# Performance work log

Measured on AMD Instinct MI355X. Metric: run time of the kernel, lower is better.

## Reference

```python
import jax, jax.numpy as jnp
import numpy as np

N = 4096          # samples
D_FEAT = 256      # embedding dim
N_CLASSES = 64
N_NEIGHBORS = 3


def _sq_dists(x):
    # torch.cdist(x, x, p=2).pow(2): squared euclidean pairwise distances
    x2 = jnp.sum(x * x, axis=1)
    d = x2[:, None] + x2[None, :] - 2.0 * (x @ x.T)
    return jnp.maximum(d, 0.0)


def setup_inputs() -> dict:
    key = jax.random.key(0)
    k1, k2 = jax.random.split(key)
    outputs = jax.random.normal(k1, (N, D_FEAT), dtype=jnp.float32)
    label_inds = jax.random.randint(k2, (N,), 0, N_CLASSES)
    return {"outputs": outputs, "label_inds": label_inds, "n_neighbors": N_NEIGHBORS}


def reference(outputs, label_inds, n_neighbors):
    n = outputs.shape[0]
    D = _sq_dists(outputs)                                    # [n, n]

    # _select_targets: per-class k-NN == masked global k-NN (same squared dists)
    same = label_inds[:, None] == label_inds[None, :]
    eye = jnp.eye(n, dtype=bool)
    dd = jnp.where(same & ~eye, D, jnp.inf)
    _, tn = jax.lax.top_k(-dd, n_neighbors)                   # [n, k] target neighbors (global idx)

    target_d = jnp.take_along_axis(D, tn, axis=1)             # [n, k]
    pull = jnp.sum(target_d)
    margin_radii = 1.0 + jnp.max(target_d, axis=1)            # [n]

    # mask: True everywhere except target neighbors and the diagonal
    rows = jnp.arange(n)[:, None]
    mask = jnp.ones((n, n), dtype=bool).at[rows, tn].set(False) & ~eye

    # Original broadcast (max_dist [n,1] vs distance [n,1,n]) yields
    #   push = sum_i sum_{a,j} relu(margin_radii[i] - D[a,j]) * mask[a,j]
    # i.e. each r_i is compared against ALL masked distances. Compute this
    # O(n^3)-element sum exactly in O(n^2 log n) via sort + prefix sums:
    #   sum_d relu(r - d) = r * #{d < r} - sum_{d < r} d
    d_flat = jnp.where(mask.reshape(-1), D.reshape(-1), jnp.inf)
    d_sorted = jnp.sort(d_flat)
    csum = jnp.cumsum(jnp.where(jnp.isinf(d_sorted), 0.0, d_sorted))
    csum0 = jnp.concatenate([jnp.zeros((1,), D.dtype), csum])
    counts = jnp.searchsorted(d_sorted, margin_radii, side='left')  # strict d < r
    push = jnp.sum(margin_radii * counts.astype(D.dtype) - csum0[counts])

    return (pull + push) / n
```

## Files before the change

### kernel.cpp

```cpp
#include <hip/hip_runtime.h>
#include <hip/hip_bf16.h>
#include <float.h>

#define N 4096
#define DF 256
#define NBINS2 4096
#define MAXM 128
#define NPUSHBLK 528

typedef __attribute__((ext_vector_type(8))) short short8v;
typedef __attribute__((ext_vector_type(8))) unsigned short ushort8v;
typedef __attribute__((ext_vector_type(4))) float floatx4;

__device__ inline unsigned short f2bf(float f) {
    __hip_bfloat16 h = __float2bfloat16(f);
    return *reinterpret_cast<unsigned short*>(&h);
}
__device__ inline float bf2f(unsigned short h) {
    unsigned int u = ((unsigned int)h) << 16;
    return __uint_as_float(u);
}

__device__ inline void gload_lds16(const void* g, void* l) {
    __builtin_amdgcn_global_load_lds((const __attribute__((address_space(1))) void*)g,
                                     (__attribute__((address_space(3))) void*)l, 16, 0, 0);
}

__global__ __launch_bounds__(256) void prep_kernel(const float* __restrict__ X,
                                                   const int* __restrict__ labels,
                                                   float* __restrict__ x2,
                                                   __hip_bfloat16* __restrict__ Xb,
                                                   int* __restrict__ cnt,
                                                   int* __restrict__ members,
                                                   double* __restrict__ accd,
                                                   int useXb) {
    int t = threadIdx.x;
    if (blockIdx.x == 1024) {
        __shared__ int scnt[64];
        if (t < 8) accd[t] = 0.0;
        if (t < 64) scnt[t] = 0;
        __syncthreads();
        for (int i = t; i < N; i += 256) {
            int c = labels[i];
            int pos = atomicAdd(&scnt[c], 1);
            if (pos < MAXM) members[(c << 8) + pos] = i;
        }
        __syncthreads();
        if (t < 64) cnt[t] = min(scnt[t], MAXM);
        return;
    }
    int row = blockIdx.x * 4 + (t >> 6);
    int l = t & 63;
    int idx = row * 64 + l;
    float4 v = ((const float4*)X)[idx];
    if (useXb) {
        ushort4 o;
        o.x = f2bf(v.x); o.y = f2bf(v.y); o.z = f2bf(v.z); o.w = f2bf(v.w);
        ((ushort4*)Xb)[idx] = o;
    }
    float s = v.x * v.x + v.y * v.y + v.z * v.z + v.w * v.w;
#pragma unroll
    for (int off = 32; off > 0; off >>= 1) s += __shfl_xor(s, off, 64);
    if (l == 0) x2[row] = s;
}

__device__ inline void top3_upd(float& b0, float& b1, float& b2, float dd) {
    if (dd < b2) {
        if (dd < b1) { b2 = b1; if (dd < b0) { b1 = b0; b0 = dd; } else b1 = dd; }
        else b2 = dd;
    }
}

__global__ __launch_bounds__(512) void knn_mfma_kernel(const float* __restrict__ X,
                                                       const float* __restrict__ x2,
                                                       const int* __restrict__ cnt,
                                                       const int* __restrict__ members,
                                                       float* __restrict__ radii,
                                                       float* __restrict__ targetd) {
    __shared__ __align__(16) char smem[131072];
    __shared__ int marr[MAXM];
    __shared__ float mx2[MAXM];

    int c = blockIdx.x;
    int m = cnt[c];
    int tid = threadIdx.x;
    int lane = tid & 63;
    int wid = tid >> 6;
    const int* mem = members + (c << 8);

    if (tid < MAXM) {
        int mi = (tid < m) ? mem[tid] : -1;
        marr[tid] = mi;
        mx2[tid] = (mi >= 0) ? x2[mi] : 0.f;
    }
    __syncthreads();

    int RB = (m + 15) >> 4;
    char* Hi = smem;
    char* Lo = smem + 65536;

    for (int idx = tid; idx < RB * 512; idx += 512) {
        int rb = idx >> 9;
        int rem = idx & 511;
        int kb = rem >> 4;
        int r0 = rem & 15;
        int row = rb * 16 + r0;
        ushort8v vhi = (ushort8v){0,0,0,0,0,0,0,0};
        ushort8v vlo = vhi;
        if (row < m) {
            const float4* src = (const float4*)(X + (size_t)marr[row] * DF + kb * 8);
            float4 u0 = src[0], u1 = src[1];
            float uu[8] = {u0.x, u0.y, u0.z, u0.w, u1.x, u1.y, u1.z, u1.w};
#pragma unroll
            for (int p = 0; p < 8; ++p) {
                unsigned short h = f2bf(uu[p]);
                vhi[p] = h;
                vlo[p] = f2bf(uu[p] - bf2f(h));
            }
        }
        *((ushort8v*)(Hi + ((size_t)idx << 4))) = vhi;
        *((ushort8v*)(Lo + ((size_t)idx << 4))) = vlo;
    }
    __syncthreads();

    if (wid >= RB) return;

    short8v aHi[8], aLo[8];
#pragma unroll
    for (int kk = 0; kk < 8; ++kk) {
        size_t off = (size_t)wid * 8192 + (size_t)kk * 1024 + ((size_t)lane << 4);
        aHi[kk] = *((const short8v*)(Hi + off));
        aLo[kk] = *((const short8v*)(Lo + off));
    }

    int g = lane >> 4;
    int cl = lane & 15;
    float x2i[4];
#pragma unroll
    for (int r = 0; r < 4; ++r) {
        int il = wid * 16 + g * 4 + r;
        x2i[r] = (il < MAXM) ? mx2[il] : 0.f;
    }

    float t0[4], t1[4], t2[4];
#pragma unroll
    for (int r = 0; r < 4; ++r) { t0[r] = FLT_MAX; t1[r] = FLT_MAX; t2[r] = FLT_MAX; }

    for (int ct = 0; ct < RB; ++ct) {
        floatx4 acc = (floatx4){0.f, 0.f, 0.f, 0.f};
#pragma unroll
        for (int kk = 0; kk < 8; ++kk) {
            size_t off = (size_t)ct * 8192 + (size_t)kk * 1024 + ((size_t)lane << 4);
            short8v bHi = *((const short8v*)(Hi + off));
            short8v bLo = *((const short8v*)(Lo + off));
            acc = __builtin_amdgcn_mfma_f32_16x16x32_bf16(aLo[kk], bHi, acc, 0, 0, 0);
            acc = __builtin_amdgcn_mfma_f32_16x16x32_bf16(aHi[kk], bLo, acc, 0, 0, 0);
            acc = __builtin_amdgcn_mfma_f32_16x16x32_bf16(aHi[kk], bHi, acc, 0, 0, 0);
        }
        int jl = ct * 16 + cl;
        float x2j = (jl < MAXM) ? mx2[jl] : 0.f;
#pragma unroll
        for (int r = 0; r < 4; ++r) {
            int il = wid * 16 + g * 4 + r;
            float d = fmaxf(x2i[r] + x2j - 2.f * acc[r], 0.f);
            bool valid = (jl < m) && (il < m) && (jl != il);
            top3_upd(t0[r], t1[r], t2[r], valid ? d : FLT_MAX);
        }
    }

#pragma unroll
    for (int off = 1; off <= 8; off <<= 1) {
#pragma unroll
        for (int r = 0; r < 4; ++r) {
            float c0 = __shfl_xor(t0[r], off, 64);
            float c1 = __shfl_xor(t1[r], off, 64);
            float c2 = __shfl_xor(t2[r], off, 64);
            float m0, m1, m2;
            if (t0[r] <= c0) {
                m0 = t0[r];
                if (t1[r] <= c0) { m1 = t1[r]; m2 = fminf(t2[r], c0); }
                else { m1 = c0; m2 = fminf(t1[r], c1); }
            } else {
                m0 = c0;
                if (c1 <= t0[r]) { m1 = c1; m2 = fminf(c2, t0[r]); }
                else { m1 = t0[r]; m2 = fminf(c1, t1[r]); }
            }
            t0[r] = m0; t1[r] = m1; t2[r] = m2;
        }
    }
    if (cl == 0) {
#pragma unroll
        for (int r = 0; r < 4; ++r) {
            int il = wid * 16 + g * 4 + r;
            if (il < m) {
                int gi = marr[il];
                targetd[3 * gi + 0] = t0[r];
                targetd[3 * gi + 1] = t1[r];
                targetd[3 * gi + 2] = t2[r];
                radii[gi] = 1.f + t2[r];
            }
        }
    }
}

__global__ __launch_bounds__(1024) void histo_ftab_kernel(const float* __restrict__ radii,
                                                          const float* __restrict__ targetd,
                                                          float2* __restrict__ ftab_g,
                                                          float* __restrict__ hdr,
                                                          double* __restrict__ accd) {
    __shared__ int cntb[NBINS2];
    __shared__ float sumb[NBINS2];
    __shared__ float fv[NBINS2 + 1];
    __shared__ float aux[64];
    __shared__ int iaux[16];
    int t = threadIdx.x;
    int wid = t >> 6, lane = t & 63;

    float4 vv = ((const float4*)radii)[t];
    float v0 = vv.x, v1 = vv.y, v2 = vv.z, v3 = vv.w;

    float mn = fminf(fminf(v0, v1), fminf(v2, v3));
    float mx = fmaxf(fmaxf(v0, v1), fmaxf(v2, v3));
#pragma unroll
    for (int off = 32; off > 0; off >>= 1) {
        mn = fminf(mn, __shfl_xor(mn, off, 64));
        mx = fmaxf(mx, __shfl_xor(mx, off, 64));
    }
    if (lane == 0) { aux[wid] = mn; aux[wid + 16] = mx; }
    cntb[t] = 0; cntb[t + 1024] = 0; cntb[t + 2048] = 0; cntb[t + 3072] = 0;
    sumb[t] = 0.f; sumb[t + 1024] = 0.f; sumb[t + 2048] = 0.f; sumb[t + 3072] = 0.f;
    __syncthreads();
    mn = aux[0]; mx = aux[16];
    for (int w = 1; w < 16; ++w) { mn = fminf(mn, aux[w]); mx = fmaxf(mx, aux[w + 16]); }
    float range = fmaxf(mx - mn, 1e-30f);
    float scale = (float)NBINS2 / range * (1.f - 1e-6f);

    int b0i = max(0, min((int)((v0 - mn) * scale), NBINS2 - 1));
    int b1i = max(0, min((int)((v1 - mn) * scale), NBINS2 - 1));
    int b2i = max(0, min((int)((v2 - mn) * scale), NBINS2 - 1));
    int b3i = max(0, min((int)((v3 - mn) * scale), NBINS2 - 1));
    atomicAdd(&cntb[b0i], 1); atomicAdd(&sumb[b0i], v0);
    atomicAdd(&cntb[b1i], 1); atomicAdd(&sumb[b1i], v1);
    atomicAdd(&cntb[b2i], 1); atomicAdd(&sumb[b2i], v2);
    atomicAdd(&cntb[b3i], 1); atomicAdd(&sumb[b3i], v3);
    __syncthreads();

    int c0 = cntb[4 * t], c1 = cntb[4 * t + 1], c2 = cntb[4 * t + 2], c3 = cntb[4 * t + 3];
    float s0 = sumb[4 * t], s1 = sumb[4 * t + 1], s2 = sumb[4 * t + 2], s3 = sumb[4 * t + 3];
    int toti = c0 + c1 + c2 + c3;
    float totf = s0 + s1 + s2 + s3;
    int sci = toti;
    float scf = totf;
#pragma unroll
    for (int off = 1; off < 64; off <<= 1) {
        int yi = __shfl_down(sci, off, 64);
        float yf = __shfl_down(scf, off, 64);
        if (lane + off < 64) { sci += yi; scf += yf; }
    }
    if (lane == 0) { iaux[wid] = sci; aux[wid] = scf; }
    __syncthreads();
    if (t < 16) {
        int xi = iaux[t];
        float xf = aux[t];
        int si = xi;
        float sf = xf;
#pragma unroll
        for (int off = 1; off < 16; off <<= 1) {
            int yi = __shfl_down(si, off, 64);
            float yf = __shfl_down(sf, off, 64);
            if (t + off < 16) { si += yi; sf += yf; }
        }
        iaux[t] = si - xi;
        aux[t] = sf - xf;
    }
    __syncthreads();
    int afteri = iaux[wid] + (sci - toti);
    float afterf = aux[wid] + (scf - totf);
    int C3 = c3 + afteri, C2 = c2 + C3, C1 = c1 + C2, C0 = c0 + C1;
    float S3 = s3 + afterf, S2 = s2 + S3, S1 = s1 + S2, S0 = s0 + S1;

    float wbin = range / (float)NBINS2;
    {
        float x0 = mn + wbin * (float)(4 * t);
        fv[4 * t + 0] = S0 - x0 * (float)C0;
        float x1 = mn + wbin * (float)(4 * t + 1);
        fv[4 * t + 1] = S1 - x1 * (float)C1;
        float x2e = mn + wbin * (float)(4 * t + 2);
        fv[4 * t + 2] = S2 - x2e * (float)C2;
        float x3 = mn + wbin * (float)(4 * t + 3);
        fv[4 * t + 3] = S3 - x3 * (float)C3;
    }
    if (t == 0) fv[NBINS2] = 0.f;
    __syncthreads();

    for (int b = t; b < NBINS2; b += 1024)
        ftab_g[b] = make_float2(fv[b], fv[b + 1] - fv[b]);
    float Stot = fv[0] + mn * (float)N;
    if (t == 0) {
        hdr[0] = mn;
        hdr[1] = mx;
        hdr[2] = (float)NBINS2 / fmaxf(mx - mn, 1e-20f);
        hdr[3] = Stot;
    }

    float invw = (float)NBINS2 / fmaxf(mx - mn, 1e-20f);
    float loc = 0.f, pul = 0.f;
    for (int idx = t; idx < 3 * N; idx += 1024) {
        float d = targetd[idx];
        pul += d;
        if (d >= mx) continue;
        if (d < mn) {
            loc += fmaf(-d, (float)N, Stot);
        } else {
            float tpos = (d - mn) * invw;
            int b = min((int)tpos, NBINS2 - 1);
            float frac = tpos - (float)b;
            loc += fmaf(frac, fv[b + 1] - fv[b], fv[b]);
        }
    }
#pragma unroll
    for (int off = 32; off > 0; off >>= 1) {
        loc += __shfl_xor(loc, off, 64);
        pul += __shfl_xor(pul, off, 64);
    }
    __syncthreads();
    if (lane == 0) { aux[wid] = loc; aux[wid + 16] = pul; }
    __syncthreads();
    if (t == 0) {
        float s = 0.f, p = 0.f;
        for (int w = 0; w < 16; ++w) { s += aux[w]; p += aux[w + 16]; }
        accd[2] = (double)s;
        accd[0] = (double)p;
    }
}

template<int USEXB>
__global__ __launch_bounds__(256) void push_gemm_kernel(const float* __restrict__ X,
                                                        const __hip_bfloat16* __restrict__ Xb,
                                                        const float* __restrict__ x2,
                                                        const float2* __restrict__ ftab_g,
                                                        const float* __restrict__ hdr,
                                                        float* __restrict__ pp) {
    __shared__ __align__(16) char smem[32768];
    __shared__ float x2r[128], x2c[128];
    __shared__ float red[256];

    int bid = blockIdx.x;
    int by = 0, rem = bid;
    while (rem >= 32 - by) { rem -= 32 - by; ++by; }
    int bx = by + rem;
    int rowBase = by * 128, colBase = bx * 128;

    int tid = threadIdx.x;
    int lane = tid & 63;
    int wv = tid >> 6;
    int wy = wv >> 1, wx = wv & 1;

    floatx4 acc4[4][4];
#pragma unroll
    for (int m = 0; m < 4; ++m)
#pragma unroll
        for (int n = 0; n < 4; ++n) acc4[m][n] = (floatx4){0.f, 0.f, 0.f, 0.f};

    if (tid < 128) { x2r[tid] = x2[rowBase + tid]; x2c[tid] = x2[colBase + tid]; }

    for (int k0 = 0; k0 < DF; k0 += 64) {
        if (k0) __syncthreads();
        if (USEXB) {
            const __hip_bfloat16* Ab = Xb + (size_t)rowBase * DF;
            const __hip_bfloat16* Bb = Xb + (size_t)colBase * DF;
#pragma unroll
            for (int i = 0; i < 4; ++i) {
                int did = wv * 256 + i * 64 + lane;
                int row = ((did >> 7) << 4) | (did & 15);
                int kb = (did >> 4) & 7;
                size_t goff = (size_t)row * DF + k0 + kb * 8;
                char* ldsA = smem + (size_t)(wv * 256 + i * 64) * 16;
                gload_lds16(Ab + goff, ldsA);
                gload_lds16(Bb + goff, ldsA + 16384);
            }
        } else {
#pragma unroll
            for (int cch = 0; cch < 4; ++cch) {
                int did = tid + (cch << 8);
                int row = ((did >> 7) << 4) | (did & 15);
                int kb = (did >> 4) & 7;
                const float* srcA = X + (size_t)(rowBase + row) * DF + k0 + kb * 8;
                const float* srcB = X + (size_t)(colBase + row) * DF + k0 + kb * 8;
                float4 a0 = *(const float4*)srcA;
                float4 a1 = *(const float4*)(srcA + 4);
                float4 e0 = *(const float4*)srcB;
                float4 e1 = *(const float4*)(srcB + 4);
                ushort8v va, vb;
                va[0] = f2bf(a0.x); va[1] = f2bf(a0.y); va[2] = f2bf(a0.z); va[3] = f2bf(a0.w);
                va[4] = f2bf(a1.x); va[5] = f2bf(a1.y); va[6] = f2bf(a1.z); va[7] = f2bf(a1.w);
                vb[0] = f2bf(e0.x); vb[1] = f2bf(e0.y); vb[2] = f2bf(e0.z); vb[3] = f2bf(e0.w);
                vb[4] = f2bf(e1.x); vb[5] = f2bf(e1.y); vb[6] = f2bf(e1.z); vb[7] = f2bf(e1.w);
                *((ushort8v*)(smem + (did << 4))) = va;
                *((ushort8v*)(smem + 16384 + (did << 4))) = vb;
            }
        }
        __syncthreads();
#pragma unroll
        for (int kk = 0; kk < 2; ++kk) {
            short8v a[4], b[4];
#pragma unroll
            for (int m = 0; m < 4; ++m)
                a[m] = *((const short8v*)(smem + (((wy * 4 + m) * 2 + kk) << 10) + (lane << 4)));
#pragma unroll
            for (int n = 0; n < 4; ++n)
                b[n] = *((const short8v*)(smem + 16384 + (((wx * 4 + n) * 2 + kk) << 10) + (lane << 4)));
#pragma unroll
            for (int m = 0; m < 4; ++m)
#pragma unroll
                for (int n = 0; n < 4; ++n)
                    acc4[m][n] = __builtin_amdgcn_mfma_f32_16x16x32_bf16(a[m], b[n], acc4[m][n], 0, 0, 0);
        }
    }
    __syncthreads();

    float4* ft4 = (float4*)smem;
    for (int i = tid; i < 2048; i += 256) ft4[i] = ((const float4*)ftab_g)[i];
    __syncthreads();
    const float2* ftab = (const float2*)smem;
    float d0v = hdr[0], rmaxv = hdr[1], invw = hdr[2], Stot = hdr[3];
    bool diag = (by == bx);

    float local = 0.f;
    int g = lane >> 4;
    int cl = lane & 15;
#pragma unroll
    for (int m = 0; m < 4; ++m) {
#pragma unroll
        for (int n = 0; n < 4; ++n) {
            floatx4 v = acc4[m][n];
            int gcl = wx * 64 + n * 16 + cl;
            float x2cv = x2c[gcl];
#pragma unroll
            for (int r = 0; r < 4; ++r) {
                int grl = wy * 64 + m * 16 + g * 4 + r;
                if (diag && grl == gcl) continue;
                float d = fmaxf(x2r[grl] + x2cv - 2.f * v[r], 0.f);
                if (d >= rmaxv) continue;
                if (d < d0v) {
                    local += fmaf(-d, (float)N, Stot);
                } else {
                    float tpos = (d - d0v) * invw;
                    int b = min((int)tpos, NBINS2 - 1);
                    float frac = tpos - (float)b;
                    float2 ab = ftab[b];
                    local += fmaf(frac, ab.y, ab.x);
                }
            }
        }
    }
    red[tid] = local;
    __syncthreads();
    for (int s2 = 128; s2 > 0; s2 >>= 1) {
        if (tid < s2) red[tid] += red[tid + s2];
        __syncthreads();
    }
    if (tid == 0) {
        float wt = diag ? 1.f : 2.f;
        pp[bid] = wt * red[0];
    }
}

__global__ __launch_bounds__(256) void finalize_kernel(const double* __restrict__ accd,
                                                       const float* __restrict__ pp,
                                                       float* __restrict__ out) {
    __shared__ double wsum[4];
    int t = threadIdx.x;
    double s = 0.0;
    for (int i = t; i < NPUSHBLK; i += 256) s += (double)pp[i];
#pragma unroll
    for (int off = 32; off > 0; off >>= 1) s += __shfl_xor(s, off, 64);
    if ((t & 63) == 0) wsum[t >> 6] = s;
    __syncthreads();
    if (t == 0) {
        double tot = wsum[0] + wsum[1] + wsum[2] + wsum[3];
        out[0] = (float)((accd[0] + tot - accd[2]) / (double)N);
    }
}

extern "C" void kernel_launch(void* const* d_in, const int* in_sizes, int n_in,
                              void* d_out, int out_size, void* d_ws, size_t ws_size,
                              hipStream_t stream) {
    const float* X = (const float*)d_in[0];
    const int* labels = (const int*)d_in[1];
    float* out = (float*)d_out;

    char* w = (char*)d_ws;
    double* accd   = (double*)w;
    float* x2      = (float*)(w + 64);
    float* radii   = (float*)(w + 64 + 16384);
    float* targetd = (float*)(w + 64 + 32768);
    int* cnt       = (int*)(w + 64 + 81920);
    int* members   = (int*)(w + 64 + 82176);
    float* hdr     = (float*)(w + 64 + 147712);
    float2* ftab_g = (float2*)(w + 64 + 147776);
    float* pp      = (float*)(w + 64 + 180544);
    __hip_bfloat16* Xb = (__hip_bfloat16*)(w + 64 + 184640);
    size_t need_xb = 64 + 184640 + (size_t)N * DF * 2;
    int useXb = (ws_size >= need_xb) ? 1 : 0;

    hipLaunchKernelGGL(prep_kernel, dim3(1025), dim3(256), 0, stream,
                       X, labels, x2, Xb, cnt, members, accd, useXb);
    hipLaunchKernelGGL(knn_mfma_kernel, dim3(64), dim3(512), 0, stream,
                       X, x2, cnt, members, radii, targetd);
    hipLaunchKernelGGL(histo_ftab_kernel, dim3(1), dim3(1024), 0, stream,
                       radii, targetd, ftab_g, hdr, accd);
    if (useXb)
        hipLaunchKernelGGL(push_gemm_kernel<1>, dim3(NPUSHBLK), dim3(256), 0, stream,
                           X, Xb, x2, ftab_g, hdr, pp);
    else
        hipLaunchKernelGGL(push_gemm_kernel<0>, dim3(NPUSHBLK), dim3(256), 0, stream,
                           X, Xb, x2, ftab_g, hdr, pp);
    hipLaunchKernelGGL(finalize_kernel, dim3(1), dim3(256), 0, stream, accd, pp, out);
}
```

Baseline: 68.92 us.

## Fuse radii histogram and lookup table build into push GEMM kernel

Drops the single-block histogram/ftab kernel and has every push GEMM block rebuild the radii histogram and prefix table in shared memory, with fewer bins and padded LDS indexing. Block 0 also computes the pull sum and the target-distance correction afterwards. This removes one serialized single-block launch and its global round-trip. In exchange, each of the 528 blocks repeats the histogram work and its atomics, and block 0 carries extra tail work. The halved bin count also changes the interpolation accuracy.

```diff
diff --git a/kernel.cpp b/kernel.cpp
--- a/kernel.cpp
+++ b/kernel.cpp
@@ -4,9 +4,10 @@
 
 #define N 4096
 #define DF 256
-#define NBINS2 4096
+#define NB 2048
 #define MAXM 128
 #define NPUSHBLK 528
+#define PAD(e) ((e) + ((e) >> 3))
 
 typedef __attribute__((ext_vector_type(8))) short short8v;
 typedef __attribute__((ext_vector_type(8))) unsigned short ushort8v;
@@ -203,147 +204,21 @@
     }
 }
 
-__global__ __launch_bounds__(1024) void histo_ftab_kernel(const float* __restrict__ radii,
-                                                          const float* __restrict__ targetd,
-                                                          float2* __restrict__ ftab_g,
-                                                          float* __restrict__ hdr,
-                                                          double* __restrict__ accd) {
-    __shared__ int cntb[NBINS2];
-    __shared__ float sumb[NBINS2];
-    __shared__ float fv[NBINS2 + 1];
-    __shared__ float aux[64];
-    __shared__ int iaux[16];
-    int t = threadIdx.x;
-    int wid = t >> 6, lane = t & 63;
-
-    float4 vv = ((const float4*)radii)[t];
-    float v0 = vv.x, v1 = vv.y, v2 = vv.z, v3 = vv.w;
-
-    float mn = fminf(fminf(v0, v1), fminf(v2, v3));
-    float mx = fmaxf(fmaxf(v0, v1), fmaxf(v2, v3));
-#pragma unroll
-    for (int off = 32; off > 0; off >>= 1) {
-        mn = fminf(mn, __shfl_xor(mn, off, 64));
-        mx = fmaxf(mx, __shfl_xor(mx, off, 64));
-    }
-    if (lane == 0) { aux[wid] = mn; aux[wid + 16] = mx; }
-    cntb[t] = 0; cntb[t + 1024] = 0; cntb[t + 2048] = 0; cntb[t + 3072] = 0;
-    sumb[t] = 0.f; sumb[t + 1024] = 0.f; sumb[t + 2048] = 0.f; sumb[t + 3072] = 0.f;
-    __syncthreads();
-    mn = aux[0]; mx = aux[16];
-    for (int w = 1; w < 16; ++w) { mn = fminf(mn, aux[w]); mx = fmaxf(mx, aux[w + 16]); }
-    float range = fmaxf(mx - mn, 1e-30f);
-    float scale = (float)NBINS2 / range * (1.f - 1e-6f);
-
-    int b0i = max(0, min((int)((v0 - mn) * scale), NBINS2 - 1));
-    int b1i = max(0, min((int)((v1 - mn) * scale), NBINS2 - 1));
-    int b2i = max(0, min((int)((v2 - mn) * scale), NBINS2 - 1));
-    int b3i = max(0, min((int)((v3 - mn) * scale), NBINS2 - 1));
-    atomicAdd(&cntb[b0i], 1); atomicAdd(&sumb[b0i], v0);
-    atomicAdd(&cntb[b1i], 1); atomicAdd(&sumb[b1i], v1);
-    atomicAdd(&cntb[b2i], 1); atomicAdd(&sumb[b2i], v2);
-    atomicAdd(&cntb[b3i], 1); atomicAdd(&sumb[b3i], v3);
-    __syncthreads();
-
-    int c0 = cntb[4 * t], c1 = cntb[4 * t + 1], c2 = cntb[4 * t + 2], c3 = cntb[4 * t + 3];
-    float s0 = sumb[4 * t], s1 = sumb[4 * t + 1], s2 = sumb[4 * t + 2], s3 = sumb[4 * t + 3];
-    int toti = c0 + c1 + c2 + c3;
-    float totf = s0 + s1 + s2 + s3;
-    int sci = toti;
-    float scf = totf;
-#pragma unroll
-    for (int off = 1; off < 64; off <<= 1) {
-        int yi = __shfl_down(sci, off, 64);
-        float yf = __shfl_down(scf, off, 64);
-        if (lane + off < 64) { sci += yi; scf += yf; }
-    }
-    if (lane == 0) { iaux[wid] = sci; aux[wid] = scf; }
-    __syncthreads();
-    if (t < 16) {
-        int xi = iaux[t];
-        float xf = aux[t];
-        int si = xi;
-        float sf = xf;
-#pragma unroll
-        for (int off = 1; off < 16; off <<= 1) {
-            int yi = __shfl_down(si, off, 64);
-            float yf = __shfl_down(sf, off, 64);
-            if (t + off < 16) { si += yi; sf += yf; }
-        }
-        iaux[t] = si - xi;
-        aux[t] = sf - xf;
-    }
-    __syncthreads();
-    int afteri = iaux[wid] + (sci - toti);
-    float afterf = aux[wid] + (scf - totf);
-    int C3 = c3 + afteri, C2 = c2 + C3, C1 = c1 + C2, C0 = c0 + C1;
-    float S3 = s3 + afterf, S2 = s2 + S3, S1 = s1 + S2, S0 = s0 + S1;
-
-    float wbin = range / (float)NBINS2;
-    {
-        float x0 = mn + wbin * (float)(4 * t);
-        fv[4 * t + 0] = S0 - x0 * (float)C0;
-        float x1 = mn + wbin * (float)(4 * t + 1);
-        fv[4 * t + 1] = S1 - x1 * (float)C1;
-        float x2e = mn + wbin * (float)(4 * t + 2);
-        fv[4 * t + 2] = S2 - x2e * (float)C2;
-        float x3 = mn + wbin * (float)(4 * t + 3);
-        fv[4 * t + 3] = S3 - x3 * (float)C3;
-    }
-    if (t == 0) fv[NBINS2] = 0.f;
-    __syncthreads();
-
-    for (int b = t; b < NBINS2; b += 1024)
-        ftab_g[b] = make_float2(fv[b], fv[b + 1] - fv[b]);
-    float Stot = fv[0] + mn * (float)N;
-    if (t == 0) {
-        hdr[0] = mn;
-        hdr[1] = mx;
-        hdr[2] = (float)NBINS2 / fmaxf(mx - mn, 1e-20f);
-        hdr[3] = Stot;
-    }
-
-    float invw = (float)NBINS2 / fmaxf(mx - mn, 1e-20f);
-    float loc = 0.f, pul = 0.f;
-    for (int idx = t; idx < 3 * N; idx += 1024) {
-        float d = targetd[idx];
-        pul += d;
-        if (d >= mx) continue;
-        if (d < mn) {
-            loc += fmaf(-d, (float)N, Stot);
-        } else {
-            float tpos = (d - mn) * invw;
-            int b = min((int)tpos, NBINS2 - 1);
-            float frac = tpos - (float)b;
-            loc += fmaf(frac, fv[b + 1] - fv[b], fv[b]);
-        }
-    }
-#pragma unroll
-    for (int off = 32; off > 0; off >>= 1) {
-        loc += __shfl_xor(loc, off, 64);
-        pul += __shfl_xor(pul, off, 64);
-    }
-    __syncthreads();
-    if (lane == 0) { aux[wid] = loc; aux[wid + 16] = pul; }
-    __syncthreads();
-    if (t == 0) {
-        float s = 0.f, p = 0.f;
-        for (int w = 0; w < 16; ++w) { s += aux[w]; p += aux[w + 16]; }
-        accd[2] = (double)s;
-        accd[0] = (double)p;
-    }
-}
-
 template<int USEXB>
 __global__ __launch_bounds__(256) void push_gemm_kernel(const float* __restrict__ X,
                                                         const __hip_bfloat16* __restrict__ Xb,
                                                         const float* __restrict__ x2,
-                                                        const float2* __restrict__ ftab_g,
-                                                        const float* __restrict__ hdr,
-                                                        float* __restrict__ pp) {
+                                                        const float* __restrict__ radii,
+                                                        const float* __restrict__ targetd,
+                                                        float* __restrict__ pp,
+                                                        double* __restrict__ accd) {
     __shared__ __align__(16) char smem[32768];
+    __shared__ __align__(16) float fvP[PAD(NB) + 2];
     __shared__ float x2r[128], x2c[128];
     __shared__ float red[256];
+    __shared__ float mmx[8];
+    __shared__ int iww[4];
+    __shared__ float fww[4];
 
     int bid = blockIdx.x;
     int by = 0, rem = bid;
@@ -356,13 +231,91 @@
     int wv = tid >> 6;
     int wy = wv >> 1, wx = wv & 1;
 
+    if (tid < 128) { x2r[tid] = x2[rowBase + tid]; x2c[tid] = x2[colBase + tid]; }
+
+    int* cntP = (int*)smem;
+    float* sumP = (float*)(smem + 9216);
+    {
+        int4 zz = {0, 0, 0, 0};
+        int4* z4 = (int4*)smem;
+        for (int i = tid; i < 1152; i += 256) z4[i] = zz;
+
+        float4 r4[4];
+#pragma unroll
+        for (int q = 0; q < 4; ++q) r4[q] = ((const float4*)radii)[tid * 4 + q];
+        float mnl = r4[0].x, mxl = r4[0].x;
+#pragma unroll
+        for (int q = 0; q < 4; ++q) {
+            mnl = fminf(mnl, fminf(fminf(r4[q].x, r4[q].y), fminf(r4[q].z, r4[q].w)));
+            mxl = fmaxf(mxl, fmaxf(fmaxf(r4[q].x, r4[q].y), fmaxf(r4[q].z, r4[q].w)));
+        }
+#pragma unroll
+        for (int off = 32; off > 0; off >>= 1) {
+            mnl = fminf(mnl, __shfl_xor(mnl, off, 64));
+            mxl = fmaxf(mxl, __shfl_xor(mxl, off, 64));
+        }
+        if (lane == 0) { mmx[wv] = mnl; mmx[4 + wv] = mxl; }
+        __syncthreads();
+    }
+    float mn = fminf(fminf(mmx[0], mmx[1]), fminf(mmx[2], mmx[3]));
+    float mx = fmaxf(fmaxf(mmx[4], mmx[5]), fmaxf(mmx[6], mmx[7]));
+    float range = fmaxf(mx - mn, 1e-30f);
+    float scale = (float)NB / range * (1.f - 1e-6f);
+    float wbin = 1.f / scale;
+    {
+        float4 r4[4];
+#pragma unroll
+        for (int q = 0; q < 4; ++q) r4[q] = ((const float4*)radii)[tid * 4 + q];
+#pragma unroll
+        for (int q = 0; q < 4; ++q) {
+            float vals[4] = {r4[q].x, r4[q].y, r4[q].z, r4[q].w};
+#pragma unroll
+            for (int p = 0; p < 4; ++p) {
+                float v = vals[p];
+                int b = max(0, min((int)((v - mn) * scale), NB - 1));
+                int pb = b + (b >> 3);
+                atomicAdd(&cntP[pb], 1);
+                atomicAdd(&sumP[pb], v);
+            }
+        }
+        __syncthreads();
+
+        int ci[8]; float si[8];
+        int Ct = 0; float St = 0.f;
+        int base = tid * 9;
+#pragma unroll
+        for (int k = 0; k < 8; ++k) {
+            ci[k] = cntP[base + k]; si[k] = sumP[base + k];
+            Ct += ci[k]; St += si[k];
+        }
+        int sci = Ct; float scf = St;
+#pragma unroll
+        for (int off = 1; off < 64; off <<= 1) {
+            int yi = __shfl_down(sci, off, 64);
+            float yf = __shfl_down(scf, off, 64);
+            if (lane + off < 64) { sci += yi; scf += yf; }
+        }
+        if (lane == 0) { iww[wv] = sci; fww[wv] = scf; }
+        __syncthreads();
+        int aC = 0; float aS = 0.f;
+        for (int w2 = wv + 1; w2 < 4; ++w2) { aC += iww[w2]; aS += fww[w2]; }
+        int runC = aC + (sci - Ct);
+        float runS = aS + (scf - St);
+#pragma unroll
+        for (int k = 7; k >= 0; --k) {
+            runC += ci[k]; runS += si[k];
+            float xe = mn + wbin * (float)(8 * tid + k);
+            fvP[base + k] = runS - xe * (float)runC;
+        }
+        if (tid == 0) fvP[PAD(NB)] = 0.f;
+        __syncthreads();
+    }
+
     floatx4 acc4[4][4];
 #pragma unroll
     for (int m = 0; m < 4; ++m)
 #pragma unroll
         for (int n = 0; n < 4; ++n) acc4[m][n] = (floatx4){0.f, 0.f, 0.f, 0.f};
-
-    if (tid < 128) { x2r[tid] = x2[rowBase + tid]; x2c[tid] = x2[colBase + tid]; }
 
     for (int k0 = 0; k0 < DF; k0 += 64) {
         if (k0) __syncthreads();
@@ -419,11 +372,7 @@
     }
     __syncthreads();
 
-    float4* ft4 = (float4*)smem;
-    for (int i = tid; i < 2048; i += 256) ft4[i] = ((const float4*)ftab_g)[i];
-    __syncthreads();
-    const float2* ftab = (const float2*)smem;
-    float d0v = hdr[0], rmaxv = hdr[1], invw = hdr[2], Stot = hdr[3];
+    float fv0 = fvP[0];
     bool diag = (by == bx);
 
     float local = 0.f;
@@ -441,15 +390,16 @@
                 int grl = wy * 64 + m * 16 + g * 4 + r;
                 if (diag && grl == gcl) continue;
                 float d = fmaxf(x2r[grl] + x2cv - 2.f * v[r], 0.f);
-                if (d >= rmaxv) continue;
-                if (d < d0v) {
-                    local += fmaf(-d, (float)N, Stot);
+                if (d >= mx) continue;
+                if (d < mn) {
+                    local += fmaf(mn - d, (float)N, fv0);
                 } else {
-                    float tpos = (d - d0v) * invw;
-                    int b = min((int)tpos, NBINS2 - 1);
+                    float tpos = (d - mn) * scale;
+                    int b = min((int)tpos, NB - 1);
                     float frac = tpos - (float)b;
-                    float2 ab = ftab[b];
-                    local += fmaf(frac, ab.y, ab.x);
+                    float fa = fvP[b + (b >> 3)];
+                    float fb = fvP[(b + 1) + ((b + 1) >> 3)];
+                    local += fmaf(frac, fb - fa, fa);
                 }
             }
         }
@@ -463,6 +413,42 @@
     if (tid == 0) {
         float wt = diag ? 1.f : 2.f;
         pp[bid] = wt * red[0];
+    }
+
+    if (bid == 0) {
+        float pul = 0.f, loc = 0.f;
+        for (int idx = tid; idx < 3 * N; idx += 256) {
+            float d = targetd[idx];
+            pul += d;
+            if (d < mx) {
+                if (d < mn) {
+                    loc += fmaf(mn - d, (float)N, fv0);
+                } else {
+                    float tpos = (d - mn) * scale;
+                    int b = min((int)tpos, NB - 1);
+                    float frac = tpos - (float)b;
+                    float fa = fvP[b + (b >> 3)];
+                    float fb = fvP[(b + 1) + ((b + 1) >> 3)];
+                    loc += fmaf(frac, fb - fa, fa);
+                }
+            }
+        }
+        __syncthreads();
+        red[tid] = pul;
+        __syncthreads();
+        for (int s2 = 128; s2 > 0; s2 >>= 1) {
+            if (tid < s2) red[tid] += red[tid + s2];
+            __syncthreads();
+        }
+        if (tid == 0) accd[0] = (double)red[0];
+        __syncthreads();
+        red[tid] = loc;
+        __syncthreads();
+        for (int s2 = 128; s2 > 0; s2 >>= 1) {
+            if (tid < s2) red[tid] += red[tid + s2];
+            __syncthreads();
+        }
+        if (tid == 0) accd[2] = (double)red[0];
     }
 }
 
@@ -497,24 +483,20 @@
     float* targetd = (float*)(w + 64 + 32768);
     int* cnt       = (int*)(w + 64 + 81920);
     int* members   = (int*)(w + 64 + 82176);
-    float* hdr     = (float*)(w + 64 + 147712);
-    float2* ftab_g = (float2*)(w + 64 + 147776);
-    float* pp      = (float*)(w + 64 + 180544);
-    __hip_bfloat16* Xb = (__hip_bfloat16*)(w + 64 + 184640);
-    size_t need_xb = 64 + 184640 + (size_t)N * DF * 2;
+    float* pp      = (float*)(w + 64 + 147712);
+    __hip_bfloat16* Xb = (__hip_bfloat16*)(w + 64 + 151808);
+    size_t need_xb = 64 + 151808 + (size_t)N * DF * 2;
     int useXb = (ws_size >= need_xb) ? 1 : 0;
 
     hipLaunchKernelGGL(prep_kernel, dim3(1025), dim3(256), 0, stream,
                        X, labels, x2, Xb, cnt, members, accd, useXb);
     hipLaunchKernelGGL(knn_mfma_kernel, dim3(64), dim3(512), 0, stream,
                        X, x2, cnt, members, radii, targetd);
-    hipLaunchKernelGGL(histo_ftab_kernel, dim3(1), dim3(1024), 0, stream,
-                       radii, targetd, ftab_g, hdr, accd);
     if (useXb)
         hipLaunchKernelGGL(push_gemm_kernel<1>, dim3(NPUSHBLK), dim3(256), 0, stream,
-                           X, Xb, x2, ftab_g, hdr, pp);
+                           X, Xb, x2, radii, targetd, pp, accd);
     else
         hipLaunchKernelGGL(push_gemm_kernel<0>, dim3(NPUSHBLK), dim3(256), 0, stream,
-                           X, Xb, x2, ftab_g, hdr, pp);
+                           X, Xb, x2, radii, targetd, pp, accd);
     hipLaunchKernelGGL(finalize_kernel, dim3(1), dim3(256), 0, stream, accd, pp, out);
 }
```

After: 79.05 us. +14.7%, slower.
